# Kernel tuning notes

Hardware: AMD Instinct MI355X
Metric: run time of the kernel (lower is better)

## Reference

```python
import jax, jax.numpy as jnp
import numpy as np

B, MEM_LEN, DEC_LEN = 8, 512, 32
MEM_H, DEC_H, H = 512, 512, 1024


def setup_inputs() -> dict:
    key = jax.random.key(0)
    ks = jax.random.split(key, 12)
    mem = jax.random.normal(ks[0], (B, MEM_LEN, MEM_H), jnp.float32)
    dec_hid = jax.random.normal(ks[1], (B, DEC_LEN, DEC_H), jnp.float32)
    mem_mask = jax.random.bernoulli(ks[2], 0.1, (B, MEM_LEN))
    dec_mask = jax.random.bernoulli(ks[3], 0.1, (B, DEC_LEN))
    dup_mask = jax.random.bernoulli(ks[4], 0.05, (B, DEC_LEN, MEM_LEN + 1))
    dup_mask = dup_mask.at[:, :, 0].set(False)  # keep terminate slot valid so no all--inf rows
    terminate_state = jax.random.normal(ks[5], (1, MEM_H), jnp.float32) * 0.05
    W_mem = jax.random.normal(ks[6], (H, MEM_H), jnp.float32) * 0.02
    b_mem = jnp.zeros((H,), jnp.float32)
    W_dec = jax.random.normal(ks[7], (H, DEC_H), jnp.float32) * 0.02
    b_dec = jnp.zeros((H,), jnp.float32)
    w_score = jax.random.normal(ks[8], (H,), jnp.float32) * 0.02
    b_score = jnp.zeros((), jnp.float32)
    return {"mem": mem, "dec_hid": dec_hid, "mem_mask": mem_mask, "dec_mask": dec_mask,
            "dup_mask": dup_mask, "terminate_state": terminate_state,
            "W_mem": W_mem, "b_mem": b_mem, "W_dec": W_dec, "b_dec": b_dec,
            "w_score": w_score, "b_score": b_score}


def reference(mem, dec_hid, mem_mask, dec_mask, dup_mask, terminate_state,
              W_mem, b_mem, W_dec, b_dec, w_score, b_score):
    b = mem.shape[0]
    neg_inf = jnp.float32(-jnp.inf)
    # prepend learned terminate state to memory; its mask slot is always valid
    term = jnp.broadcast_to(terminate_state[None], (b, 1, terminate_state.shape[-1]))
    mem_full = jnp.concatenate([term, mem], axis=1)                      # [B, M+1, MEM_H]
    mem_mask_full = jnp.concatenate(
        [jnp.zeros((b, 1), dtype=mem_mask.dtype), mem_mask], axis=1)     # [B, M+1]
    # project once, then broadcast-add (equivalent to Linear on expanded tensors)
    pm = jnp.einsum('bmk,hk->bmh', mem_full, W_mem) + b_mem              # [B, M+1, H]
    pd = jnp.einsum('bdk,hk->bdh', dec_hid, W_dec) + b_dec               # [B, D, H]
    h = jnp.tanh(pm[:, None, :, :] + pd[:, :, None, :])                  # [B, D, M+1, H]
    score = jnp.einsum('bdmh,h->bdm', h, w_score) + b_score              # [B, D, M+1]
    score = jnp.where(mem_mask_full[:, None, :], neg_inf, score)
    # dup_mask rows where dec step is padding are cleared (dup_mask[dec_mask,:]=0)
    dup = jnp.where(dec_mask[:, :, None], False, dup_mask)
    score = jnp.where(dup, neg_inf, score)
    return jax.nn.log_softmax(score, axis=-1)
```

## Files before the change

kernel.cpp:

```cpp
#include <hip/hip_runtime.h>
#include <hip/hip_bf16.h>
#include <math.h>

#define B 8
#define MEM_LEN 512
#define DEC_LEN 32
#define HDIM 1024
#define M1 513
#define PM_ROWS (B * M1)
#define AROWS 4224

#define NEG_BIG (-1e30f)
#define C2F 2.885390081777927f

#if __has_builtin(__builtin_amdgcn_exp2f)
#define EXP2(x) __builtin_amdgcn_exp2f(x)
#else
#define EXP2(x) exp2f(x)
#endif
#define RCP(x) __builtin_amdgcn_rcpf(x)
#define SCHED_FENCE() __builtin_amdgcn_sched_barrier(0)

typedef __bf16 bfv8 __attribute__((ext_vector_type(8)));
typedef float  f4   __attribute__((ext_vector_type(4)));
typedef float  f8   __attribute__((ext_vector_type(8)));

#define N_MF  (AROWS * 512 / 8)
#define N_DEC (256 * 512 / 8)
#define N_W   (1024 * 512 / 8)
#define N_CVT (N_MF + N_DEC + 2 * N_W)

__global__ __launch_bounds__(256) void convert_all(
        const float* __restrict__ mem, const float* __restrict__ term,
        const float* __restrict__ dec_hid,
        const float* __restrict__ W_mem, const float* __restrict__ W_dec,
        __bf16* __restrict__ mfb, __bf16* __restrict__ decb,
        __bf16* __restrict__ wmb, __bf16* __restrict__ wdb) {
    int idx = blockIdx.x * 256 + threadIdx.x;
    float4 v0 = make_float4(0.f, 0.f, 0.f, 0.f), v1 = v0;
    float scale = 1.f;
    __bf16* dst;
    if (idx < N_MF) {
        int row = idx >> 6;
        int c8  = idx & 63;
        dst = mfb + (size_t)idx * 8;
        if (row < PM_ROWS) {
            int b = row / M1, m = row - b * M1;
            const float* src = (m == 0) ? (term + c8 * 8)
                                        : (mem + ((size_t)(b * MEM_LEN + m - 1)) * 512 + c8 * 8);
            v0 = ((const float4*)src)[0];
            v1 = ((const float4*)src)[1];
        }
    } else if (idx < N_MF + N_DEC) {
        int j = idx - N_MF;
        dst = decb + (size_t)j * 8;
        v0 = ((const float4*)dec_hid)[j * 2];
        v1 = ((const float4*)dec_hid)[j * 2 + 1];
    } else if (idx < N_MF + N_DEC + N_W) {
        int j = idx - N_MF - N_DEC;
        dst = wmb + (size_t)j * 8;
        v0 = ((const float4*)W_mem)[j * 2];
        v1 = ((const float4*)W_mem)[j * 2 + 1];
        scale = C2F;
    } else {
        int j = idx - N_MF - N_DEC - N_W;
        dst = wdb + (size_t)j * 8;
        v0 = ((const float4*)W_dec)[j * 2];
        v1 = ((const float4*)W_dec)[j * 2 + 1];
        scale = C2F;
    }
    bfv8 o;
    o[0] = (__bf16)(v0.x * scale); o[1] = (__bf16)(v0.y * scale);
    o[2] = (__bf16)(v0.z * scale); o[3] = (__bf16)(v0.w * scale);
    o[4] = (__bf16)(v1.x * scale); o[5] = (__bf16)(v1.y * scale);
    o[6] = (__bf16)(v1.z * scale); o[7] = (__bf16)(v1.w * scale);
    *(bfv8*)dst = o;
}

__global__ __launch_bounds__(256, 4) void gemm_ls(
        const __bf16* __restrict__ mfb, const __bf16* __restrict__ decb,
        const __bf16* __restrict__ wmb, const __bf16* __restrict__ wdb,
        const float* __restrict__ b_mem, const float* __restrict__ b_dec,
        __bf16* __restrict__ pmb, float* __restrict__ pdf) {
    __shared__ __align__(16) __bf16 Als[2][64 * 64];
    __shared__ __align__(16) __bf16 Bls[2][64 * 64];

    int orig = blockIdx.x;
    int wg   = (orig & 7) * 140 + (orig >> 3);
    int bx   = wg >> 4;
    int by   = wg & 15;

    bool isMem = bx < 66;
    const __bf16* A  = isMem ? mfb : decb;
    const __bf16* Wb = isMem ? wmb : wdb;
    const float* bsel = isMem ? b_mem : b_dec;
    int row0 = isMem ? bx * 64 : (bx - 66) * 64;
    int n0b  = by * 64;

    int t = threadIdx.x;
    int r0 = t >> 3,          g0 = t & 7;
    int r1 = (t + 256) >> 3,  g1 = t & 7;
    int ds0 = r0 * 128 + ((g0 ^ (r0 & 7)) << 4);
    int ds1 = r1 * 128 + ((g1 ^ (r1 & 7)) << 4);
    const __bf16* aSrc0 = A  + (size_t)(row0 + r0) * 512 + g0 * 8;
    const __bf16* aSrc1 = A  + (size_t)(row0 + r1) * 512 + g1 * 8;
    const __bf16* bSrc0 = Wb + (size_t)(n0b + r0) * 512 + g0 * 8;
    const __bf16* bSrc1 = Wb + (size_t)(n0b + r1) * 512 + g1 * 8;

    int w = t >> 6, l = t & 63;
    int m0w = (w >> 1) * 32, n0w = (w & 1) * 32;
    int lr = l & 15, lq = l >> 4;

    f4 acc[2][2] = {};

    {
        bfv8 a0 = *(const bfv8*)(aSrc0);
        bfv8 a1 = *(const bfv8*)(aSrc1);
        bfv8 b0 = *(const bfv8*)(bSrc0);
        bfv8 b1 = *(const bfv8*)(bSrc1);
        *(bfv8*)((char*)&Als[0][0] + ds0) = a0;
        *(bfv8*)((char*)&Als[0][0] + ds1) = a1;
        *(bfv8*)((char*)&Bls[0][0] + ds0) = b0;
        *(bfv8*)((char*)&Bls[0][0] + ds1) = b1;
    }
    __syncthreads();

    #pragma unroll
    for (int kt = 0; kt < 8; ++kt) {
        const int cur = kt & 1;
        bfv8 na0, na1, nb0, nb1;
        if (kt < 7) {
            const int kn = (kt + 1) * 64;
            na0 = *(const bfv8*)(aSrc0 + kn);
            na1 = *(const bfv8*)(aSrc1 + kn);
            nb0 = *(const bfv8*)(bSrc0 + kn);
            nb1 = *(const bfv8*)(bSrc1 + kn);
        }
        SCHED_FENCE();
        bfv8 aF[2][2], bF[2][2];
        #pragma unroll
        for (int kk = 0; kk < 2; ++kk) {
            int g = kk * 4 + lq;
            #pragma unroll
            for (int i = 0; i < 2; ++i) {
                int rA = m0w + i * 16 + lr;
                aF[kk][i] = *(const bfv8*)((char*)&Als[cur][0] + rA * 128 + ((g ^ (rA & 7)) << 4));
                int rB = n0w + i * 16 + lr;
                bF[kk][i] = *(const bfv8*)((char*)&Bls[cur][0] + rB * 128 + ((g ^ (rB & 7)) << 4));
            }
        }
        #pragma unroll
        for (int kk = 0; kk < 2; ++kk) {
            acc[0][0] = __builtin_amdgcn_mfma_f32_16x16x32_bf16(aF[kk][0], bF[kk][0], acc[0][0], 0, 0, 0);
            acc[0][1] = __builtin_amdgcn_mfma_f32_16x16x32_bf16(aF[kk][0], bF[kk][1], acc[0][1], 0, 0, 0);
            acc[1][0] = __builtin_amdgcn_mfma_f32_16x16x32_bf16(aF[kk][1], bF[kk][0], acc[1][0], 0, 0, 0);
            acc[1][1] = __builtin_amdgcn_mfma_f32_16x16x32_bf16(aF[kk][1], bF[kk][1], acc[1][1], 0, 0, 0);
        }
        if (kt < 7) {
            const int nxt = cur ^ 1;
            *(bfv8*)((char*)&Als[nxt][0] + ds0) = na0;
            *(bfv8*)((char*)&Als[nxt][0] + ds1) = na1;
            *(bfv8*)((char*)&Bls[nxt][0] + ds0) = nb0;
            *(bfv8*)((char*)&Bls[nxt][0] + ds1) = nb1;
        }
        __syncthreads();
    }

    int crow = lq * 4;
    int ccol = lr;
    #pragma unroll
    for (int j = 0; j < 2; ++j) {
        int col = n0b + n0w + j * 16 + ccol;
        float bv = bsel[col] * C2F;
        #pragma unroll
        for (int i = 0; i < 2; ++i) {
            #pragma unroll
            for (int r = 0; r < 4; ++r) {
                int row = row0 + m0w + i * 16 + crow + r;
                float e = EXP2(acc[i][j][r] + bv);
                if (isMem) pmb[(size_t)row * HDIM + col] = (__bf16)e;
                else       pdf[(size_t)row * HDIM + col] = e;
            }
        }
    }
}

__global__ __launch_bounds__(256, 4) void score8(
        const __bf16* __restrict__ pm, const float* __restrict__ pdf,
        const float* __restrict__ w_score,
        const unsigned char* __restrict__ mem_mask,
        const unsigned char* __restrict__ dec_mask,
        const unsigned char* __restrict__ dup_mask,
        float* __restrict__ sc) {
    __shared__ float pdl[4][HDIM];
    int bid = blockIdx.x;
    int b    = bid & 7;
    int rest = bid >> 3;
    int dg   = rest & 7;
    int mc   = rest >> 3;
    int t = threadIdx.x, w = t >> 6, l = t & 63;
    int bd0 = b * DEC_LEN + dg * 4;

    {
        int d  = t >> 6;
        int h0 = (t & 63) * 16;
        const f4* src = (const f4*)(pdf + (size_t)(bd0 + d) * HDIM + h0);
        f4* dst = (f4*)&pdl[d][h0];
        dst[0] = src[0]; dst[1] = src[1]; dst[2] = src[2]; dst[3] = src[3];
    }

    f8 w22[2];
    float sumw_l = 0.f;
    #pragma unroll
    for (int half = 0; half < 2; ++half) {
        f8 wv = *(const f8*)(w_score + half * 512 + l * 8);
        #pragma unroll
        for (int j = 0; j < 8; ++j) {
            sumw_l += wv[j];
            w22[half][j] = wv[j] * 2.f;
        }
    }
    #pragma unroll
    for (int off = 32; off; off >>= 1) sumw_l += __shfl_xor(sumw_l, off, 64);
    float sumw_all = sumw_l;

    bool dm[4];
    #pragma unroll
    for (int d = 0; d < 4; ++d) dm[d] = dec_mask[bd0 + d] != 0;
    const unsigned char* dup0 = dup_mask + (size_t)bd0 * M1;

    __syncthreads();

    int mbase = mc * 32 + w * 8;
    for (int i = 0; i < 8; ++i) {
        int m = mbase + i;
        if (m >= M1) break;
        bool memm = (m > 0) && (mem_mask[b * MEM_LEN + m - 1] != 0);
        if (memm) {
            if (l == 0) {
                #pragma unroll
                for (int d = 0; d < 4; ++d)
                    sc[(size_t)(bd0 + d) * M1 + m] = NEG_BIG;
            }
            continue;
        }
        const __bf16* pmr = pm + ((size_t)(b * M1 + m)) * HDIM + l * 8;
        bfv8 p0 = *(const bfv8*)(pmr);
        bfv8 p1 = *(const bfv8*)(pmr + 512);
        f8 pf0, pf1;
        #pragma unroll
        for (int j = 0; j < 8; ++j) { pf0[j] = (float)p0[j]; pf1[j] = (float)p1[j]; }
        float ac[4] = {};
        #pragma unroll
        for (int d = 0; d < 4; ++d) {
            f4 q0a = *(const f4*)&pdl[d][l * 8];
            f4 q0b = *(const f4*)&pdl[d][l * 8 + 4];
            f4 q1a = *(const f4*)&pdl[d][512 + l * 8];
            f4 q1b = *(const f4*)&pdl[d][512 + l * 8 + 4];
            #pragma unroll
            for (int j = 0; j < 4; ++j) {
                float t0 = fmaf(pf0[j],     q0a[j], 1.f);
                float t1 = fmaf(pf0[j + 4], q0b[j], 1.f);
                float t2 = fmaf(pf1[j],     q1a[j], 1.f);
                float t3 = fmaf(pf1[j + 4], q1b[j], 1.f);
                float D01 = t0 * t1;
                float D23 = t2 * t3;
                float N01 = fmaf(w22[0][j], t1, w22[0][j + 4] * t0);
                float N23 = fmaf(w22[1][j], t3, w22[1][j + 4] * t2);
                float N   = fmaf(N01, D23, N23 * D01);
                float D   = D01 * D23;
                ac[d] = fmaf(N, RCP(D), ac[d]);
            }
        }
        float a0 = ac[0], a1 = ac[1], a2 = ac[2], a3 = ac[3];
        #pragma unroll
        for (int off = 32; off; off >>= 1) {
            a0 += __shfl_xor(a0, off, 64);
            a1 += __shfl_xor(a1, off, 64);
            a2 += __shfl_xor(a2, off, 64);
            a3 += __shfl_xor(a3, off, 64);
        }
        float s[4];
        s[0] = sumw_all - a0;
        s[1] = sumw_all - a1;
        s[2] = sumw_all - a2;
        s[3] = sumw_all - a3;
        #pragma unroll
        for (int d = 0; d < 4; ++d) {
            bool kill = (!dm[d] && dup0[(size_t)d * M1 + m]);
            s[d] = kill ? NEG_BIG : s[d];
        }
        if (l == 0) {
            #pragma unroll
            for (int d = 0; d < 4; ++d)
                sc[(size_t)(bd0 + d) * M1 + m] = s[d];
        }
    }
}

__global__ __launch_bounds__(512) void softmax_k(const float* __restrict__ sc,
                                                 float* __restrict__ out) {
    __shared__ float red[512];
    int bd = blockIdx.x, t = threadIdx.x;
    const float* row = sc + (size_t)bd * M1;
    float v = row[t];
    float v512 = row[512];
    float lm = (t == 0) ? fmaxf(v, v512) : v;
    red[t] = lm;
    __syncthreads();
    for (int s = 256; s > 0; s >>= 1) {
        if (t < s) red[t] = fmaxf(red[t], red[t + s]);
        __syncthreads();
    }
    float mx = red[0];
    __syncthreads();
    float le = __expf(v - mx);
    if (t == 0) le += __expf(v512 - mx);
    red[t] = le;
    __syncthreads();
    for (int s = 256; s > 0; s >>= 1) {
        if (t < s) red[t] += red[t + s];
        __syncthreads();
    }
    float lse = mx + __logf(red[0]);
    float* orow = out + (size_t)bd * M1;
    orow[t] = v - lse;
    if (t == 0) orow[512] = v512 - lse;
}

extern "C" void kernel_launch(void* const* d_in, const int* in_sizes, int n_in,
                              void* d_out, int out_size, void* d_ws, size_t ws_size,
                              hipStream_t stream) {
    const float* mem      = (const float*)d_in[0];
    const float* dec_hid  = (const float*)d_in[1];
    const unsigned char* mem_mask = (const unsigned char*)d_in[2];
    const unsigned char* dec_mask = (const unsigned char*)d_in[3];
    const unsigned char* dup_mask = (const unsigned char*)d_in[4];
    const float* term     = (const float*)d_in[5];
    const float* W_mem    = (const float*)d_in[6];
    const float* b_mem    = (const float*)d_in[7];
    const float* W_dec    = (const float*)d_in[8];
    const float* b_dec    = (const float*)d_in[9];
    const float* w_score  = (const float*)d_in[10];

    float* out = (float*)d_out;
    char* ws = (char*)d_ws;
    __bf16* mfb  = (__bf16*)ws;
    __bf16* decb = mfb + (size_t)AROWS * 512;
    __bf16* wmb  = decb + (size_t)256 * 512;
    __bf16* wdb  = wmb + (size_t)1024 * 512;
    __bf16* pmb  = wdb + (size_t)1024 * 512;
    float*  pdf  = (float*)(pmb + (size_t)AROWS * HDIM);
    float*  sc   = pdf + (size_t)256 * HDIM;

    convert_all<<<N_CVT / 256, 256, 0, stream>>>(mem, term, dec_hid, W_mem, W_dec,
                                                 mfb, decb, wmb, wdb);
    gemm_ls<<<1120, 256, 0, stream>>>(mfb, decb, wmb, wdb, b_mem, b_dec, pmb, pdf);
    score8<<<8 * 8 * 17, 256, 0, stream>>>(pmb, pdf, w_score,
                                           mem_mask, dec_mask, dup_mask, sc);
    softmax_k<<<B * DEC_LEN, 512, 0, stream>>>(sc, out);
}
```

Measured before the change: 50.11 us.

## Enlarge projection GEMM tiles to 128x128 with 4x4 MFMA per wave

```diff
diff --git a/kernel.cpp b/kernel.cpp
--- a/kernel.cpp
+++ b/kernel.cpp
@@ -77,91 +77,88 @@
     *(bfv8*)dst = o;
 }
 
-__global__ __launch_bounds__(256, 4) void gemm_ls(
+__global__ __launch_bounds__(256, 2) void gemm_ls(
         const __bf16* __restrict__ mfb, const __bf16* __restrict__ decb,
         const __bf16* __restrict__ wmb, const __bf16* __restrict__ wdb,
         const float* __restrict__ b_mem, const float* __restrict__ b_dec,
         __bf16* __restrict__ pmb, float* __restrict__ pdf) {
-    __shared__ __align__(16) __bf16 Als[2][64 * 64];
-    __shared__ __align__(16) __bf16 Bls[2][64 * 64];
+    __shared__ __align__(16) __bf16 Als[2][128 * 64];
+    __shared__ __align__(16) __bf16 Bls[2][128 * 64];
 
     int orig = blockIdx.x;
-    int wg   = (orig & 7) * 140 + (orig >> 3);
-    int bx   = wg >> 4;
-    int by   = wg & 15;
-
-    bool isMem = bx < 66;
+    int wg   = (orig & 7) * 35 + (orig >> 3);
+    int bx   = wg >> 3;
+    int by   = wg & 7;
+
+    bool isMem = bx < 33;
     const __bf16* A  = isMem ? mfb : decb;
     const __bf16* Wb = isMem ? wmb : wdb;
     const float* bsel = isMem ? b_mem : b_dec;
-    int row0 = isMem ? bx * 64 : (bx - 66) * 64;
-    int n0b  = by * 64;
+    int row0 = isMem ? bx * 128 : (bx - 33) * 128;
+    int n0b  = by * 128;
 
     int t = threadIdx.x;
-    int r0 = t >> 3,          g0 = t & 7;
-    int r1 = (t + 256) >> 3,  g1 = t & 7;
-    int ds0 = r0 * 128 + ((g0 ^ (r0 & 7)) << 4);
-    int ds1 = r1 * 128 + ((g1 ^ (r1 & 7)) << 4);
-    const __bf16* aSrc0 = A  + (size_t)(row0 + r0) * 512 + g0 * 8;
-    const __bf16* aSrc1 = A  + (size_t)(row0 + r1) * 512 + g1 * 8;
-    const __bf16* bSrc0 = Wb + (size_t)(n0b + r0) * 512 + g0 * 8;
-    const __bf16* bSrc1 = Wb + (size_t)(n0b + r1) * 512 + g1 * 8;
+    int rb = t >> 3, g0 = t & 7;
+    int ds0 = rb * 128 + ((g0 ^ (rb & 7)) << 4);
+    const __bf16* aS = A  + (size_t)(row0 + rb) * 512 + g0 * 8;
+    const __bf16* bS = Wb + (size_t)(n0b + rb) * 512 + g0 * 8;
 
     int w = t >> 6, l = t & 63;
-    int m0w = (w >> 1) * 32, n0w = (w & 1) * 32;
+    int m0w = (w >> 1) * 64, n0w = (w & 1) * 64;
     int lr = l & 15, lq = l >> 4;
 
-    f4 acc[2][2] = {};
+    f4 acc[4][4] = {};
 
     {
-        bfv8 a0 = *(const bfv8*)(aSrc0);
-        bfv8 a1 = *(const bfv8*)(aSrc1);
-        bfv8 b0 = *(const bfv8*)(bSrc0);
-        bfv8 b1 = *(const bfv8*)(bSrc1);
-        *(bfv8*)((char*)&Als[0][0] + ds0) = a0;
-        *(bfv8*)((char*)&Als[0][0] + ds1) = a1;
-        *(bfv8*)((char*)&Bls[0][0] + ds0) = b0;
-        *(bfv8*)((char*)&Bls[0][0] + ds1) = b1;
+        #pragma unroll
+        for (int p = 0; p < 4; ++p) {
+            bfv8 a = *(const bfv8*)(aS + p * 16384);
+            bfv8 b = *(const bfv8*)(bS + p * 16384);
+            *(bfv8*)((char*)&Als[0][0] + ds0 + p * 4096) = a;
+            *(bfv8*)((char*)&Bls[0][0] + ds0 + p * 4096) = b;
+        }
     }
     __syncthreads();
 
     #pragma unroll
     for (int kt = 0; kt < 8; ++kt) {
         const int cur = kt & 1;
-        bfv8 na0, na1, nb0, nb1;
+        bfv8 na[4], nb[4];
         if (kt < 7) {
             const int kn = (kt + 1) * 64;
-            na0 = *(const bfv8*)(aSrc0 + kn);
-            na1 = *(const bfv8*)(aSrc1 + kn);
-            nb0 = *(const bfv8*)(bSrc0 + kn);
-            nb1 = *(const bfv8*)(bSrc1 + kn);
+            #pragma unroll
+            for (int p = 0; p < 4; ++p) {
+                na[p] = *(const bfv8*)(aS + p * 16384 + kn);
+                nb[p] = *(const bfv8*)(bS + p * 16384 + kn);
+            }
         }
         SCHED_FENCE();
-        bfv8 aF[2][2], bF[2][2];
+        bfv8 aF[2][4], bF[2][4];
         #pragma unroll
         for (int kk = 0; kk < 2; ++kk) {
-            int g = kk * 4 + lq;
-            #pragma unroll
-            for (int i = 0; i < 2; ++i) {
+            int gk = kk * 4 + lq;
+            #pragma unroll
+            for (int i = 0; i < 4; ++i) {
                 int rA = m0w + i * 16 + lr;
-                aF[kk][i] = *(const bfv8*)((char*)&Als[cur][0] + rA * 128 + ((g ^ (rA & 7)) << 4));
+                aF[kk][i] = *(const bfv8*)((char*)&Als[cur][0] + rA * 128 + ((gk ^ (rA & 7)) << 4));
                 int rB = n0w + i * 16 + lr;
-                bF[kk][i] = *(const bfv8*)((char*)&Bls[cur][0] + rB * 128 + ((g ^ (rB & 7)) << 4));
-            }
-        }
-        #pragma unroll
-        for (int kk = 0; kk < 2; ++kk) {
-            acc[0][0] = __builtin_amdgcn_mfma_f32_16x16x32_bf16(aF[kk][0], bF[kk][0], acc[0][0], 0, 0, 0);
-            acc[0][1] = __builtin_amdgcn_mfma_f32_16x16x32_bf16(aF[kk][0], bF[kk][1], acc[0][1], 0, 0, 0);
-            acc[1][0] = __builtin_amdgcn_mfma_f32_16x16x32_bf16(aF[kk][1], bF[kk][0], acc[1][0], 0, 0, 0);
-            acc[1][1] = __builtin_amdgcn_mfma_f32_16x16x32_bf16(aF[kk][1], bF[kk][1], acc[1][1], 0, 0, 0);
-        }
+                bF[kk][i] = *(const bfv8*)((char*)&Bls[cur][0] + rB * 128 + ((gk ^ (rB & 7)) << 4));
+            }
+        }
+        #pragma unroll
+        for (int kk = 0; kk < 2; ++kk)
+            #pragma unroll
+            for (int i = 0; i < 4; ++i)
+                #pragma unroll
+                for (int j = 0; j < 4; ++j)
+                    acc[i][j] = __builtin_amdgcn_mfma_f32_16x16x32_bf16(aF[kk][i], bF[kk][j], acc[i][j], 0, 0, 0);
         if (kt < 7) {
             const int nxt = cur ^ 1;
-            *(bfv8*)((char*)&Als[nxt][0] + ds0) = na0;
-            *(bfv8*)((char*)&Als[nxt][0] + ds1) = na1;
-            *(bfv8*)((char*)&Bls[nxt][0] + ds0) = nb0;
-            *(bfv8*)((char*)&Bls[nxt][0] + ds1) = nb1;
+            #pragma unroll
+            for (int p = 0; p < 4; ++p) {
+                *(bfv8*)((char*)&Als[nxt][0] + ds0 + p * 4096) = na[p];
+                *(bfv8*)((char*)&Bls[nxt][0] + ds0 + p * 4096) = nb[p];
+            }
         }
         __syncthreads();
     }
@@ -169,11 +166,11 @@
     int crow = lq * 4;
     int ccol = lr;
     #pragma unroll
-    for (int j = 0; j < 2; ++j) {
+    for (int j = 0; j < 4; ++j) {
         int col = n0b + n0w + j * 16 + ccol;
         float bv = bsel[col] * C2F;
         #pragma unroll
-        for (int i = 0; i < 2; ++i) {
+        for (int i = 0; i < 4; ++i) {
             #pragma unroll
             for (int r = 0; r < 4; ++r) {
                 int row = row0 + m0w + i * 16 + crow + r;
@@ -355,7 +352,7 @@
 
     convert_all<<<N_CVT / 256, 256, 0, stream>>>(mem, term, dec_hid, W_mem, W_dec,
                                                  mfb, decb, wmb, wdb);
-    gemm_ls<<<1120, 256, 0, stream>>>(mfb, decb, wmb, wdb, b_mem, b_dec, pmb, pdf);
+    gemm_ls<<<280, 256, 0, stream>>>(mfb, decb, wmb, wdb, b_mem, b_dec, pmb, pdf);
     score8<<<8 * 8 * 17, 256, 0, stream>>>(pmb, pdf, w_score,
                                            mem_mask, dec_mask, dup_mask, sc);
     softmax_k<<<B * DEC_LEN, 512, 0, stream>>>(sc, out);
```

Result: slower. 51.68 us (+3.1%).

## Score 8 decoder steps per block and prefetch next memory row

Applied to the files above, without the earlier changes.

```diff
diff --git a/kernel.cpp b/kernel.cpp
--- a/kernel.cpp
+++ b/kernel.cpp
@@ -185,28 +185,29 @@
     }
 }
 
-__global__ __launch_bounds__(256, 4) void score8(
+__global__ __launch_bounds__(256, 4) void score9(
         const __bf16* __restrict__ pm, const float* __restrict__ pdf,
         const float* __restrict__ w_score,
         const unsigned char* __restrict__ mem_mask,
         const unsigned char* __restrict__ dec_mask,
         const unsigned char* __restrict__ dup_mask,
         float* __restrict__ sc) {
-    __shared__ float pdl[4][HDIM];
+    __shared__ float pdl[8][HDIM];
     int bid = blockIdx.x;
     int b    = bid & 7;
     int rest = bid >> 3;
-    int dg   = rest & 7;
-    int mc   = rest >> 3;
+    int dg   = rest & 3;
+    int mc   = rest >> 2;
     int t = threadIdx.x, w = t >> 6, l = t & 63;
-    int bd0 = b * DEC_LEN + dg * 4;
+    int bd0 = b * DEC_LEN + dg * 8;
 
     {
-        int d  = t >> 6;
-        int h0 = (t & 63) * 16;
+        int d  = t >> 5;
+        int h0 = (t & 31) * 32;
         const f4* src = (const f4*)(pdf + (size_t)(bd0 + d) * HDIM + h0);
         f4* dst = (f4*)&pdl[d][h0];
-        dst[0] = src[0]; dst[1] = src[1]; dst[2] = src[2]; dst[3] = src[3];
+        #pragma unroll
+        for (int q = 0; q < 8; ++q) dst[q] = src[q];
     }
 
     f8 w22[2];
@@ -224,77 +225,87 @@
     for (int off = 32; off; off >>= 1) sumw_l += __shfl_xor(sumw_l, off, 64);
     float sumw_all = sumw_l;
 
-    bool dm[4];
-    #pragma unroll
-    for (int d = 0; d < 4; ++d) dm[d] = dec_mask[bd0 + d] != 0;
+    bool dm[8];
+    #pragma unroll
+    for (int d = 0; d < 8; ++d) dm[d] = dec_mask[bd0 + d] != 0;
     const unsigned char* dup0 = dup_mask + (size_t)bd0 * M1;
 
     __syncthreads();
 
     int mbase = mc * 32 + w * 8;
+    int rowm[8];
+    bool rv[8], msk[8];
+    #pragma unroll
     for (int i = 0; i < 8; ++i) {
         int m = mbase + i;
-        if (m >= M1) break;
-        bool memm = (m > 0) && (mem_mask[b * MEM_LEN + m - 1] != 0);
-        if (memm) {
+        rv[i]   = (m < M1);
+        rowm[i] = rv[i] ? m : 0;
+        msk[i]  = (rowm[i] > 0) && (mem_mask[b * MEM_LEN + rowm[i] - 1] != 0);
+    }
+
+    const __bf16* pmbase = pm + (size_t)(b * M1) * HDIM + l * 8;
+    bfv8 p0c = *(const bfv8*)(pmbase + (size_t)rowm[0] * HDIM);
+    bfv8 p1c = *(const bfv8*)(pmbase + (size_t)rowm[0] * HDIM + 512);
+
+    #pragma unroll
+    for (int i = 0; i < 8; ++i) {
+        bfv8 p0n, p1n;
+        if (i < 7) {
+            p0n = *(const bfv8*)(pmbase + (size_t)rowm[i + 1] * HDIM);
+            p1n = *(const bfv8*)(pmbase + (size_t)rowm[i + 1] * HDIM + 512);
+        }
+        SCHED_FENCE();
+        int m = rowm[i];
+        if (msk[i]) {
             if (l == 0) {
                 #pragma unroll
-                for (int d = 0; d < 4; ++d)
+                for (int d = 0; d < 8; ++d)
                     sc[(size_t)(bd0 + d) * M1 + m] = NEG_BIG;
             }
-            continue;
-        }
-        const __bf16* pmr = pm + ((size_t)(b * M1 + m)) * HDIM + l * 8;
-        bfv8 p0 = *(const bfv8*)(pmr);
-        bfv8 p1 = *(const bfv8*)(pmr + 512);
-        f8 pf0, pf1;
-        #pragma unroll
-        for (int j = 0; j < 8; ++j) { pf0[j] = (float)p0[j]; pf1[j] = (float)p1[j]; }
-        float ac[4] = {};
-        #pragma unroll
-        for (int d = 0; d < 4; ++d) {
-            f4 q0a = *(const f4*)&pdl[d][l * 8];
-            f4 q0b = *(const f4*)&pdl[d][l * 8 + 4];
-            f4 q1a = *(const f4*)&pdl[d][512 + l * 8];
-            f4 q1b = *(const f4*)&pdl[d][512 + l * 8 + 4];
-            #pragma unroll
-            for (int j = 0; j < 4; ++j) {
-                float t0 = fmaf(pf0[j],     q0a[j], 1.f);
-                float t1 = fmaf(pf0[j + 4], q0b[j], 1.f);
-                float t2 = fmaf(pf1[j],     q1a[j], 1.f);
-                float t3 = fmaf(pf1[j + 4], q1b[j], 1.f);
-                float D01 = t0 * t1;
-                float D23 = t2 * t3;
-                float N01 = fmaf(w22[0][j], t1, w22[0][j + 4] * t0);
-                float N23 = fmaf(w22[1][j], t3, w22[1][j + 4] * t2);
-                float N   = fmaf(N01, D23, N23 * D01);
-                float D   = D01 * D23;
-                ac[d] = fmaf(N, RCP(D), ac[d]);
-            }
-        }
-        float a0 = ac[0], a1 = ac[1], a2 = ac[2], a3 = ac[3];
-        #pragma unroll
-        for (int off = 32; off; off >>= 1) {
-            a0 += __shfl_xor(a0, off, 64);
-            a1 += __shfl_xor(a1, off, 64);
-            a2 += __shfl_xor(a2, off, 64);
-            a3 += __shfl_xor(a3, off, 64);
-        }
-        float s[4];
-        s[0] = sumw_all - a0;
-        s[1] = sumw_all - a1;
-        s[2] = sumw_all - a2;
-        s[3] = sumw_all - a3;
-        #pragma unroll
-        for (int d = 0; d < 4; ++d) {
-            bool kill = (!dm[d] && dup0[(size_t)d * M1 + m]);
-            s[d] = kill ? NEG_BIG : s[d];
-        }
-        if (l == 0) {
-            #pragma unroll
-            for (int d = 0; d < 4; ++d)
-                sc[(size_t)(bd0 + d) * M1 + m] = s[d];
-        }
+        } else {
+            f8 pf0, pf1;
+            #pragma unroll
+            for (int j = 0; j < 8; ++j) { pf0[j] = (float)p0c[j]; pf1[j] = (float)p1c[j]; }
+            float ac[8];
+            #pragma unroll
+            for (int d = 0; d < 8; ++d) ac[d] = 0.f;
+            #pragma unroll
+            for (int d = 0; d < 8; ++d) {
+                f4 q0a = *(const f4*)&pdl[d][l * 8];
+                f4 q0b = *(const f4*)&pdl[d][l * 8 + 4];
+                f4 q1a = *(const f4*)&pdl[d][512 + l * 8];
+                f4 q1b = *(const f4*)&pdl[d][512 + l * 8 + 4];
+                #pragma unroll
+                for (int j = 0; j < 4; ++j) {
+                    float t0 = fmaf(pf0[j],     q0a[j], 1.f);
+                    float t1 = fmaf(pf0[j + 4], q0b[j], 1.f);
+                    float t2 = fmaf(pf1[j],     q1a[j], 1.f);
+                    float t3 = fmaf(pf1[j + 4], q1b[j], 1.f);
+                    float D01 = t0 * t1;
+                    float D23 = t2 * t3;
+                    float N01 = fmaf(w22[0][j], t1, w22[0][j + 4] * t0);
+                    float N23 = fmaf(w22[1][j], t3, w22[1][j + 4] * t2);
+                    float N   = fmaf(N01, D23, N23 * D01);
+                    float D   = D01 * D23;
+                    ac[d] = fmaf(N, RCP(D), ac[d]);
+                }
+            }
+            #pragma unroll
+            for (int off = 32; off; off >>= 1) {
+                #pragma unroll
+                for (int d = 0; d < 8; ++d)
+                    ac[d] += __shfl_xor(ac[d], off, 64);
+            }
+            if (l == 0 && rv[i]) {
+                #pragma unroll
+                for (int d = 0; d < 8; ++d) {
+                    float s = sumw_all - ac[d];
+                    bool kill = (!dm[d] && dup0[(size_t)d * M1 + m]);
+                    sc[(size_t)(bd0 + d) * M1 + m] = kill ? NEG_BIG : s;
+                }
+            }
+        }
+        p0c = p0n; p1c = p1n;
     }
 }
 
@@ -356,7 +367,7 @@
     convert_all<<<N_CVT / 256, 256, 0, stream>>>(mem, term, dec_hid, W_mem, W_dec,
                                                  mfb, decb, wmb, wdb);
     gemm_ls<<<1120, 256, 0, stream>>>(mfb, decb, wmb, wdb, b_mem, b_dec, pmb, pdf);
-    score8<<<8 * 8 * 17, 256, 0, stream>>>(pmb, pdf, w_score,
+    score9<<<8 * 4 * 17, 256, 0, stream>>>(pmb, pdf, w_score,
                                            mem_mask, dec_mask, dup_mask, sc);
     softmax_k<<<B * DEC_LEN, 512, 0, stream>>>(sc, out);
 }
```

After: 59.20 us. 18.1% more time.
